# Performance work log

Measured on AMD Instinct MI355X. Metric: run time of the kernel, lower is better.

## Reference

```python
import jax, jax.numpy as jnp
import numpy as np

B, T, E, H = 256, 256, 64, 4  # batch, num_trees, embedding_size, hidden_size


def setup_inputs() -> dict:
    key = jax.random.key(0)
    k1, k2, k3 = jax.random.split(key, 3)
    x = jax.random.normal(k1, (B, 1, T, E), dtype=jnp.float32)
    W1 = jax.random.normal(k2, (T, T, E, H), dtype=jnp.float32) * 0.01  # linear1 (leading 1 dropped)
    b1 = jnp.zeros((T, T, H), dtype=jnp.float32)
    W2 = jax.random.normal(k3, (T, (T - 1) * H, E), dtype=jnp.float32) * 0.01  # linear2
    b2 = jnp.zeros((T, E), dtype=jnp.float32)
    return {"x": x, "W1": W1, "b1": b1, "W2": W2, "b2": b2}


def _offdiag_idx(num_trees):
    # For each output tree i, the column indices j != i (static, shape [T, T-1]).
    mask = ~np.eye(num_trees, dtype=bool)
    return jnp.asarray(np.nonzero(mask)[1].reshape(num_trees, num_trees - 1))


def reference(x, W1, b1, W2, b2):
    num_trees, hidden = W1.shape[0], W1.shape[-1]
    x0 = x[:, 0]  # (B, T, E): broadcast dim removed; x[b,0,j,e] pairs with W1[i,j,e,h]
    # Locally-connected layer 1: per-pair (i,j) contraction over embedding dim e.
    h = jax.nn.relu(jnp.einsum('bje,ijeh->bijh', x0, W1) + b1)  # (B, T, T, H)
    # Dropout(p=0.5) is identity in eval mode.
    # masked_select(~eye): drop the diagonal j == i via a static gather.
    idx = _offdiag_idx(num_trees)  # (T, T-1)
    h2 = jnp.take_along_axis(h, idx[None, :, :, None], axis=2)  # (B, T, T-1, H)
    h2 = h2.reshape(h.shape[0], num_trees, (num_trees - 1) * hidden)
    # Locally-connected layer 2: per-tree i contraction over the (T-1)*H dim.
    out = jnp.einsum('btk,tke->bte', h2, W2) + b2  # (B, T, E)
    return out
```

## Files before the change

kernel.cpp:

```cpp
#include <hip/hip_runtime.h>


namespace {

constexpr int T_ = 256;
constexpr int E_ = 64;
constexpr int K2_ = 1020;

typedef float  f32x4  __attribute__((ext_vector_type(4)));
typedef short  bf16x8 __attribute__((ext_vector_type(8)));
typedef unsigned short u16x4 __attribute__((ext_vector_type(4)));

__device__ inline unsigned short f2b(float f) {
    union { float f; unsigned u; } v; v.f = f;
    unsigned r = v.u + 0x7fffu + ((v.u >> 16) & 1u);
    return (unsigned short)(r >> 16);
}

__device__ inline bf16x8 pack8(f32x4 a, f32x4 b) {
    bf16x8 r;
    r[0] = (short)f2b(a[0]); r[1] = (short)f2b(a[1]);
    r[2] = (short)f2b(a[2]); r[3] = (short)f2b(a[3]);
    r[4] = (short)f2b(b[0]); r[5] = (short)f2b(b[1]);
    r[6] = (short)f2b(b[2]); r[7] = (short)f2b(b[3]);
    return r;
}

constexpr int JC = 4;
constexpr int CHUNKS = 16;
constexpr int W1_ROW   = 72;
constexpr int W1_PLANE = 32 * W1_ROW + 8;
constexpr int PB_ROW   = 24;
constexpr int PB_PLANE = 64 * PB_ROW + 8;
constexpr int W2_ROW   = 16;
constexpr int W2_PLANE = 64 * W2_ROW + 8;

}


__global__ __launch_bounds__(256) void xcast_kernel(
    const float* __restrict__ x, unsigned short* __restrict__ xT)
{
    const int g     = blockIdx.x * 256 + threadIdx.x;
    const int part  = g & 3;
    const int rowid = g >> 2;
    const int b = rowid >> 8, j = rowid & 255;
    const float* src = x + (size_t)rowid * E_ + part * 16;
    f32x4 v0 = *(const f32x4*)(src);
    f32x4 v1 = *(const f32x4*)(src + 4);
    f32x4 v2 = *(const f32x4*)(src + 8);
    f32x4 v3 = *(const f32x4*)(src + 12);
    unsigned short* dst = xT + ((size_t)j * 256 + b) * E_ + part * 16;
    *(bf16x8*)(dst)     = pack8(v0, v1);
    *(bf16x8*)(dst + 8) = pack8(v2, v3);
}

__global__ __launch_bounds__(256) void init_out_kernel(
    const float* __restrict__ b2, float* __restrict__ out)
{
    const int idx = blockIdx.x * 256 + threadIdx.x;
    ((f32x4*)out)[idx] = ((const f32x4*)b2)[idx & 4095];
}


__global__ __launch_bounds__(512, 2) void w2z_kernel(
    const float* __restrict__ W2, unsigned short* __restrict__ W2Z)
{
    __shared__ __align__(16) unsigned short sT[64][136];
    const int bid = blockIdx.x;
    const int t = bid >> 3, kb = bid & 7;
    const int tid = threadIdx.x;
    {
        const int kl = tid >> 2;
        const int e0 = (tid & 3) << 4;
        const int k  = kb * 128 + kl;
        const int j  = k >> 2, h = k & 3;
        f32x4 v0 = {0,0,0,0}, v1 = {0,0,0,0}, v2 = {0,0,0,0}, v3 = {0,0,0,0};
        if (j != t) {
            const int ksrc = ((j < t) ? j : j - 1) * 4 + h;
            const float* src = W2 + ((size_t)t * K2_ + ksrc) * E_ + e0;
            v0 = *(const f32x4*)(src);
            v1 = *(const f32x4*)(src + 4);
            v2 = *(const f32x4*)(src + 8);
            v3 = *(const f32x4*)(src + 12);
        }
        #pragma unroll
        for (int m = 0; m < 4; ++m) {
            sT[e0 + m     ][kl] = f2b(v0[m]);
            sT[e0 + 4 + m ][kl] = f2b(v1[m]);
            sT[e0 + 8 + m ][kl] = f2b(v2[m]);
            sT[e0 + 12 + m][kl] = f2b(v3[m]);
        }
    }
    __syncthreads();
    {
        const int e  = tid >> 3;
        const int ko = tid & 7;
        const unsigned short* srow = &sT[e][ko * 16];
        bf16x8 a = *(const bf16x8*)(srow);
        bf16x8 b = *(const bf16x8*)(srow + 8);
        unsigned short* dst = W2Z + ((size_t)t * 64 + e) * 1024 + kb * 128 + ko * 16;
        *(bf16x8*)(dst)     = a;
        *(bf16x8*)(dst + 8) = b;
    }
}

__global__ __launch_bounds__(256, 4) void phaseA4_kernel(
    const unsigned short* __restrict__ xT,
    const float* __restrict__ W1,
    const float* __restrict__ b1,
    unsigned short* __restrict__ H,
    int i_gbase)
{
    __shared__ __align__(16) unsigned short sA[4][2][16][68];
    __shared__ __align__(16) unsigned short sH[4][4][64][8];

    const int bx = blockIdx.x;
    const int jq = ((bx & 7) << 3) | (bx >> 3);
    const int it = blockIdx.y;
    const int bh = blockIdx.z;

    const int tid = threadIdx.x;
    const int w = tid >> 6, lane = tid & 63, r16 = lane & 15, kg = lane >> 4;
    const int jp = w & 1, bq = w >> 1;
    const int bG = bh * 128 + bq * 64;
    const int jbase = jq * 4 + jp * 2;

    bf16x8 xf[2][4][2];
    #pragma unroll
    for (int jl = 0; jl < 2; ++jl)
        #pragma unroll
        for (int nt = 0; nt < 4; ++nt) {
            const unsigned short* xr =
                xT + ((size_t)(jbase + jl) * 256 + bG + nt * 16 + r16) * 64 + kg * 8;
            xf[jl][nt][0] = *(const bf16x8*)(xr);
            xf[jl][nt][1] = *(const bf16x8*)(xr + 32);
        }

    const int s_jl = lane >> 5, s_il = (lane >> 3) & 3, s_seg = lane & 7;

    for (int iq = 0; iq < 4; ++iq) {
        {
            const int ig = i_gbase + it * 16 + iq * 4 + s_il;
            const float* src = W1 + (((size_t)ig * 256 + (jbase + s_jl)) << 8) + s_seg * 32;
            f32x4 v[8];
            #pragma unroll
            for (int s4 = 0; s4 < 8; ++s4) v[s4] = *(const f32x4*)(src + s4 * 4);
            #pragma unroll
            for (int h = 0; h < 4; ++h) {
                bf16x8 pk;
                #pragma unroll
                for (int s4 = 0; s4 < 8; ++s4) pk[s4] = (short)f2b(v[s4][h]);
                *(bf16x8*)&sA[w][s_jl][s_il * 4 + h][s_seg * 8] = pk;
            }
        }
        asm volatile("s_waitcnt lgkmcnt(0)" ::: "memory");
        __builtin_amdgcn_sched_barrier(0);

        {
            bf16x8 a[2][2];
            f32x4 bias[2];
            const int igk = i_gbase + it * 16 + iq * 4 + kg;
            #pragma unroll
            for (int jl = 0; jl < 2; ++jl) {
                const unsigned short* ar = &sA[w][jl][r16][0];
                a[jl][0] = *(const bf16x8*)(ar + kg * 8);
                a[jl][1] = *(const bf16x8*)(ar + 32 + kg * 8);
                bias[jl] = *(const f32x4*)(b1 + (((size_t)igk << 8) + (jbase + jl)) * 4);
            }
            #pragma unroll
            for (int nt = 0; nt < 4; ++nt) {
                unsigned pk[4];
                #pragma unroll
                for (int jl = 0; jl < 2; ++jl) {
                    f32x4 acc = (f32x4){0.f, 0.f, 0.f, 0.f};
                    acc = __builtin_amdgcn_mfma_f32_16x16x32_bf16(a[jl][0], xf[jl][nt][0], acc, 0, 0, 0);
                    acc = __builtin_amdgcn_mfma_f32_16x16x32_bf16(a[jl][1], xf[jl][nt][1], acc, 0, 0, 0);
                    float v0 = acc[0] + bias[jl][0]; v0 = v0 > 0.f ? v0 : 0.f;
                    float v1 = acc[1] + bias[jl][1]; v1 = v1 > 0.f ? v1 : 0.f;
                    float v2 = acc[2] + bias[jl][2]; v2 = v2 > 0.f ? v2 : 0.f;
                    float v3 = acc[3] + bias[jl][3]; v3 = v3 > 0.f ? v3 : 0.f;
                    pk[jl * 2]     = (unsigned)f2b(v0) | ((unsigned)f2b(v1) << 16);
                    pk[jl * 2 + 1] = (unsigned)f2b(v2) | ((unsigned)f2b(v3) << 16);
                }
                uint4 q4; q4.x = pk[0]; q4.y = pk[1]; q4.z = pk[2]; q4.w = pk[3];
                *(uint4*)&sH[w][kg][nt * 16 + r16][0] = q4;
            }
        }
        asm volatile("s_waitcnt lgkmcnt(0)" ::: "memory");
        __builtin_amdgcn_sched_barrier(0);

        {
            const int ib = it * 16 + iq * 4;
            #pragma unroll
            for (int il = 0; il < 4; ++il) {
                bf16x8 v = *(const bf16x8*)&sH[w][il][lane][0];
                *(bf16x8*)(H + (((((size_t)(ib + il)) * 64 + jq) * 2 + jp) * 256 + bG + lane) * 8) = v;
            }
        }
    }
}

__global__ __launch_bounds__(512, 4) void phaseB_kernel(
    const unsigned short* __restrict__ H,
    const unsigned short* __restrict__ W2Z,
    const float* __restrict__ b2,
    float* __restrict__ out,
    int i_base)
{
    __shared__ __align__(16) unsigned short sA[2][128][72];
    __shared__ __align__(16) unsigned short sB[2][64][72];

    const int bid = blockIdx.x;
    const int t_loc = bid >> 1;
    const int t  = i_base + t_loc;
    const int b0 = (bid & 1) << 7;
    const int tid = threadIdx.x;
    const int w = tid >> 6, lane = tid & 63, r16 = lane & 15, kg = lane >> 4;

    auto stageA = [&](int c, int pb) {
        #pragma unroll
        for (int half = 0; half < 2; ++half) {
            const int idx = half * 512 + tid;
            const int b   = idx & 127;
            const int jp  = (idx >> 7) & 1;
            const int jql = (idx >> 8) & 3;
            const unsigned short* src =
                H + ((size_t)t_loc << 18) +
                ((size_t)((((4 * c + jql) * 2 + jp) * 256) + b0 + b) << 3);
            bf16x8 v = *(const bf16x8*)src;
            *(bf16x8*)&sA[pb][b][jql * 16 + jp * 8] = v;
        }
    };
    auto stageB = [&](int c, int pb) {
        const int e = tid >> 3;
        const int q = tid & 7;
        bf16x8 v = *(const bf16x8*)(W2Z + ((size_t)t * 64 + e) * 1024 + c * 64 + q * 8);
        *(bf16x8*)&sB[pb][e][q * 8] = v;
    };

    stageA(0, 0); stageB(0, 0);
    __syncthreads();

    f32x4 acc[4];
    #pragma unroll
    for (int nt = 0; nt < 4; ++nt) acc[nt] = (f32x4){0.f, 0.f, 0.f, 0.f};

    for (int c = 0; c < 16; ++c) {
        const int pb = c & 1;
        if (c + 1 < 16) { stageA(c + 1, pb ^ 1); stageB(c + 1, pb ^ 1); }

        const unsigned short* ar = &sA[pb][w * 16 + r16][0];
        bf16x8 a0 = *(const bf16x8*)(ar + kg * 8);
        bf16x8 a1 = *(const bf16x8*)(ar + 32 + kg * 8);
        #pragma unroll
        for (int nt = 0; nt < 4; ++nt) {
            const unsigned short* br = &sB[pb][nt * 16 + r16][0];
            bf16x8 bb0 = *(const bf16x8*)(br + kg * 8);
            bf16x8 bb1 = *(const bf16x8*)(br + 32 + kg * 8);
            acc[nt] = __builtin_amdgcn_mfma_f32_16x16x32_bf16(a0, bb0, acc[nt], 0, 0, 0);
            acc[nt] = __builtin_amdgcn_mfma_f32_16x16x32_bf16(a1, bb1, acc[nt], 0, 0, 0);
        }
        __syncthreads();
    }

    #pragma unroll
    for (int nt = 0; nt < 4; ++nt) {
        const int e = nt * 16 + r16;
        const float bias = b2[(t << 6) + e];
        #pragma unroll
        for (int r = 0; r < 4; ++r) {
            const int b = b0 + w * 16 + kg * 4 + r;
            out[((size_t)b << 14) + (t << 6) + e] = acc[nt][r] + bias;
        }
    }
}


template <bool XBF>
__global__ __launch_bounds__(512, 4) void fused_forest_kernel(
    const void*  __restrict__ xv,
    const float* __restrict__ W1,
    const float* __restrict__ b1,
    const float* __restrict__ W2,
    float* __restrict__ out)
{
    __shared__ __align__(16) unsigned short sW1[4 * W1_PLANE];
    __shared__ __align__(16) unsigned short sPB[8 * PB_PLANE];
    __shared__ __align__(16) unsigned short sW2[2][8 * W2_PLANE];
    __shared__ __align__(16) float sB1[4][32];

    const int bid = blockIdx.x;
    const int xcd = bid & 7;
    const int rr  = bid >> 3;
    const int tgl = rr >> 4;
    const int bg  = (rr >> 2) & 3;
    const int jg  = rr & 3;
    const int tg  = tgl * 8 + xcd;
    const int i0  = tg << 3;
    const int b0  = bg << 6;
    const int j0g = jg << 6;

    const int tid  = threadIdx.x;
    const int w    = tid >> 6;
    const int lane = tid & 63;
    const int r16  = lane & 15;
    const int kg   = lane >> 4;
    const int bt   = w & 3;
    const int mh   = w >> 2;

    f32x4 acc[4][4];
    #pragma unroll
    for (int mt = 0; mt < 4; ++mt)
        #pragma unroll
        for (int nt = 0; nt < 4; ++nt)
            acc[mt][nt] = (f32x4){0.f, 0.f, 0.f, 0.f};

    auto stage = [&](int c, int pb) {
        const int j0 = j0g + c * JC;
        if (tid < 128) {
            const int jj = tid >> 5, ih = tid & 31;
            sB1[jj][ih] = b1[((i0 + (ih >> 2)) * T_ + (j0 + jj)) * 4 + (ih & 3)];
        }
        {
            const float* src = W1 + (((size_t)(i0 + w) * T_ + (j0 + kg)) * E_) * 4 + r16 * 16;
            f32x4 v0 = *(const f32x4*)(src);
            f32x4 v1 = *(const f32x4*)(src + 4);
            f32x4 v2 = *(const f32x4*)(src + 8);
            f32x4 v3 = *(const f32x4*)(src + 12);
            #pragma unroll
            for (int h = 0; h < 4; ++h) {
                u16x4 pk = (u16x4){f2b(v0[h]), f2b(v1[h]), f2b(v2[h]), f2b(v3[h])};
                *(u16x4*)&sW1[kg * W1_PLANE + (w * 4 + h) * W1_ROW + r16 * 4] = pk;
            }
        }
        {
            const int kk   = lane >> 2;
            const int e0   = (lane & 3) * 16;
            const int tabs = i0 + w;
            const int j    = j0 + (kk >> 2);
            unsigned short* dst = &sW2[pb][w * W2_PLANE + kk];
            if (j == tabs) {
                #pragma unroll
                for (int q = 0; q < 16; ++q) dst[(e0 + q) * W2_ROW] = 0;
            } else {
                const int ksrc = ((j < tabs) ? j : j - 1) * 4 + (kk & 3);
                const float* src = W2 + ((size_t)tabs * K2_ + ksrc) * E_ + e0;
                f32x4 v0 = *(const f32x4*)(src);
                f32x4 v1 = *(const f32x4*)(src + 4);
                f32x4 v2 = *(const f32x4*)(src + 8);
                f32x4 v3 = *(const f32x4*)(src + 12);
                #pragma unroll
                for (int q = 0; q < 4; ++q) {
                    dst[(e0 + q)      * W2_ROW] = f2b(v0[q]);
                    dst[(e0 + 4 + q)  * W2_ROW] = f2b(v1[q]);
                    dst[(e0 + 8 + q)  * W2_ROW] = f2b(v2[q]);
                    dst[(e0 + 12 + q) * W2_ROW] = f2b(v3[q]);
                }
            }
        }
    };

    stage(0, 0);
    __syncthreads();

    const int brow = b0 + bt * 16 + r16;

    for (int c = 0; c < CHUNKS; ++c) {
        const int j0 = j0g + c * JC;
        #pragma unroll
        for (int jj = 0; jj < JC; ++jj) {
            bf16x8 xa, xc;
            if (XBF) {
                const unsigned short* xr =
                    (const unsigned short*)xv + ((size_t)(j0 + jj) * 256 + brow) * E_;
                xa = *(const bf16x8*)(xr + kg * 8);
                xc = *(const bf16x8*)(xr + 32 + kg * 8);
            } else {
                const float* xr = (const float*)xv + ((size_t)brow * T_ + (j0 + jj)) * E_ + kg * 8;
                xa = pack8(*(const f32x4*)xr, *(const f32x4*)(xr + 4));
                xc = pack8(*(const f32x4*)(xr + 32), *(const f32x4*)(xr + 36));
            }
            const unsigned short* wr = &sW1[jj * W1_PLANE + (mh * 16 + r16) * W1_ROW];
            bf16x8 wa = *(const bf16x8*)(wr + kg * 8);
            bf16x8 wc = *(const bf16x8*)(wr + 32 + kg * 8);
            f32x4 cf = (f32x4){0.f, 0.f, 0.f, 0.f};
            cf = __builtin_amdgcn_mfma_f32_16x16x32_bf16(wa, xa, cf, 0, 0, 0);
            cf = __builtin_amdgcn_mfma_f32_16x16x32_bf16(wc, xc, cf, 0, 0, 0);
            const int i = mh * 4 + kg;
            f32x4 bias = *(const f32x4*)&sB1[jj][i * 4];
            #pragma unroll
            for (int r = 0; r < 4; ++r) {
                float vv = cf[r] + bias[r];
                cf[r] = vv > 0.f ? vv : 0.f;
            }
            unsigned p0 = (unsigned)f2b(cf[0]) | ((unsigned)f2b(cf[1]) << 16);
            unsigned p1 = (unsigned)f2b(cf[2]) | ((unsigned)f2b(cf[3]) << 16);
            uint2 pk; pk.x = p0; pk.y = p1;
            *(uint2*)&sPB[i * PB_PLANE + (bt * 16 + r16) * PB_ROW + jj * 4] = pk;
        }
        __syncthreads();

        {
            const bf16x8 z = (bf16x8){0,0,0,0,0,0,0,0};
            const bool lo = (kg < 2);
            bf16x8 a2[4], bb[4];
            #pragma unroll
            for (int mt = 0; mt < 4; ++mt)
                a2[mt] = lo ? *(const bf16x8*)&sPB[w * PB_PLANE + (mt * 16 + r16) * PB_ROW + kg * 8] : z;
            #pragma unroll
            for (int nt = 0; nt < 4; ++nt)
                bb[nt] = lo ? *(const bf16x8*)&sW2[c & 1][w * W2_PLANE + (nt * 16 + r16) * W2_ROW + kg * 8] : z;
            #pragma unroll
            for (int mt = 0; mt < 4; ++mt)
                #pragma unroll
                for (int nt = 0; nt < 4; ++nt)
                    acc[mt][nt] = __builtin_amdgcn_mfma_f32_16x16x32_bf16(
                        a2[mt], bb[nt], acc[mt][nt], 0, 0, 0);
        }

        if (c + 1 < CHUNKS) stage(c + 1, (c + 1) & 1);
        __syncthreads();
    }

    const int tabs = i0 + w;
    #pragma unroll
    for (int mt = 0; mt < 4; ++mt) {
        const int b = b0 + mt * 16 + kg * 4;
        #pragma unroll
        for (int nt = 0; nt < 4; ++nt) {
            const int e = nt * 16 + r16;
            #pragma unroll
            for (int r = 0; r < 4; ++r)
                unsafeAtomicAdd(&out[((size_t)(b + r) * T_ + tabs) * E_ + e],
                                acc[mt][nt][r]);
        }
    }
}


extern "C" void kernel_launch(void* const* d_in, const int* in_sizes, int n_in,
                              void* d_out, int out_size, void* d_ws, size_t ws_size,
                              hipStream_t stream) {
    const float* x  = (const float*)d_in[0];
    const float* W1 = (const float*)d_in[1];
    const float* b1 = (const float*)d_in[2];
    const float* W2 = (const float*)d_in[3];
    const float* b2 = (const float*)d_in[4];
    float* out = (float*)d_out;
    (void)in_sizes; (void)n_in; (void)out_size;

    const size_t xT_b   = 8388608ull;
    const size_t w2z_b  = 33554432ull;
    const size_t H_full = 134217728ull;

    int NS = 0;
    if (d_ws) {
        const int cands[4] = {1, 2, 4, 8};
        for (int ci = 0; ci < 4; ++ci) {
            if (ws_size >= xT_b + w2z_b + H_full / cands[ci]) { NS = cands[ci]; break; }
        }
    }

    if (NS) {
        unsigned short* xT  = (unsigned short*)d_ws;
        unsigned short* W2Z = (unsigned short*)((char*)d_ws + xT_b);
        unsigned short* H   = (unsigned short*)((char*)d_ws + xT_b + w2z_b);

        hipLaunchKernelGGL(xcast_kernel, dim3(1024), dim3(256), 0, stream, x, xT);
        hipLaunchKernelGGL(w2z_kernel, dim3(2048), dim3(512), 0, stream, W2, W2Z);

        const int TS = 256 / NS;
        const int n_it = TS / 16;
        for (int s = 0; s < NS; ++s) {
            hipLaunchKernelGGL(phaseA4_kernel, dim3(64, n_it, 2), dim3(256), 0, stream,
                               xT, W1, b1, H, s * TS);
            hipLaunchKernelGGL(phaseB_kernel, dim3(TS * 2), dim3(512), 0, stream,
                               H, W2Z, b2, out, s * TS);
        }
    } else {
        const bool xbf = d_ws && ws_size >= xT_b;
        hipLaunchKernelGGL(init_out_kernel, dim3(4096), dim3(256), 0, stream, b2, out);
        if (xbf) {
            hipLaunchKernelGGL(xcast_kernel, dim3(1024), dim3(256), 0, stream,
                               x, (unsigned short*)d_ws);
            hipLaunchKernelGGL(fused_forest_kernel<true>, dim3(512), dim3(512), 0, stream,
                               (const void*)d_ws, W1, b1, W2, out);
        } else {
            hipLaunchKernelGGL(fused_forest_kernel<false>, dim3(512), dim3(512), 0, stream,
                               (const void*)x, W1, b1, W2, out);
        }
    }
}
```

Measured before the change: 128.8 us.

## Share W1 tile across waves with double-buffered LDS and prefetch in phase A

Phase A now loads each W1 block into a shared LDS buffer used by all four waves, instead of each wave loading its own copy. It double-buffers that buffer and issues the next iq's global loads before the MFMA work, so load latency overlaps compute. Bias is staged once in LDS, and H is written straight from registers, dropping the sH staging round-trip. In exchange it adds block-wide barriers each iteration and writes H with a less coalesced pattern.

```diff
diff --git a/kernel.cpp b/kernel.cpp
--- a/kernel.cpp
+++ b/kernel.cpp
@@ -105,26 +105,32 @@
     }
 }
 
-__global__ __launch_bounds__(256, 4) void phaseA4_kernel(
+__global__ __launch_bounds__(256, 4) void phaseA6_kernel(
     const unsigned short* __restrict__ xT,
     const float* __restrict__ W1,
     const float* __restrict__ b1,
     unsigned short* __restrict__ H,
     int i_gbase)
 {
-    __shared__ __align__(16) unsigned short sA[4][2][16][68];
-    __shared__ __align__(16) unsigned short sH[4][4][64][8];
+    __shared__ __align__(16) unsigned short sA[2][4][16][72];
+    __shared__ __align__(16) float sB1[16][16];
 
     const int bx = blockIdx.x;
     const int jq = ((bx & 7) << 3) | (bx >> 3);
     const int it = blockIdx.y;
     const int bh = blockIdx.z;
+    const int j0 = jq * 4;
 
     const int tid = threadIdx.x;
     const int w = tid >> 6, lane = tid & 63, r16 = lane & 15, kg = lane >> 4;
     const int jp = w & 1, bq = w >> 1;
     const int bG = bh * 128 + bq * 64;
-    const int jbase = jq * 4 + jp * 2;
+    const int jbase = j0 + jp * 2;
+
+    {
+        const int i = tid >> 4, f = tid & 15;
+        sB1[i][f] = b1[(((size_t)(i_gbase + it * 16 + i)) * 256 + j0) * 4 + f];
+    }
 
     bf16x8 xf[2][4][2];
     #pragma unroll
@@ -137,37 +143,47 @@
             xf[jl][nt][1] = *(const bf16x8*)(xr + 32);
         }
 
-    const int s_jl = lane >> 5, s_il = (lane >> 3) & 3, s_seg = lane & 7;
-
+    const int p_s = tid >> 4, seg = tid & 15;
+    const int il_s = p_s >> 2, jW = p_s & 3;
+
+    f32x4 r[4];
+    auto issue = [&](int iq) {
+        const float* src = W1 +
+            ((((size_t)(i_gbase + it * 16 + iq * 4 + il_s)) * 256 + (j0 + jW)) << 8) + seg * 16;
+        #pragma unroll
+        for (int s = 0; s < 4; ++s) r[s] = *(const f32x4*)(src + s * 4);
+    };
+    auto packwrite = [&](int buf) {
+        #pragma unroll
+        for (int h = 0; h < 4; ++h) {
+            u16x4 pk = (u16x4){f2b(r[0][h]), f2b(r[1][h]), f2b(r[2][h]), f2b(r[3][h])};
+            *(u16x4*)&sA[buf][jW][il_s * 4 + h][seg * 4] = pk;
+        }
+    };
+
+    issue(0);
+    packwrite(0);
+    issue(1);
+    asm volatile("s_waitcnt lgkmcnt(0)" ::: "memory");
+    __builtin_amdgcn_sched_barrier(0);
+    __builtin_amdgcn_s_barrier();
+    __builtin_amdgcn_sched_barrier(0);
+
+    #pragma unroll
     for (int iq = 0; iq < 4; ++iq) {
-        {
-            const int ig = i_gbase + it * 16 + iq * 4 + s_il;
-            const float* src = W1 + (((size_t)ig * 256 + (jbase + s_jl)) << 8) + s_seg * 32;
-            f32x4 v[8];
-            #pragma unroll
-            for (int s4 = 0; s4 < 8; ++s4) v[s4] = *(const f32x4*)(src + s4 * 4);
-            #pragma unroll
-            for (int h = 0; h < 4; ++h) {
-                bf16x8 pk;
-                #pragma unroll
-                for (int s4 = 0; s4 < 8; ++s4) pk[s4] = (short)f2b(v[s4][h]);
-                *(bf16x8*)&sA[w][s_jl][s_il * 4 + h][s_seg * 8] = pk;
-            }
-        }
-        asm volatile("s_waitcnt lgkmcnt(0)" ::: "memory");
-        __builtin_amdgcn_sched_barrier(0);
+        const int buf = iq & 1;
 
         {
             bf16x8 a[2][2];
             f32x4 bias[2];
-            const int igk = i_gbase + it * 16 + iq * 4 + kg;
             #pragma unroll
             for (int jl = 0; jl < 2; ++jl) {
-                const unsigned short* ar = &sA[w][jl][r16][0];
+                const unsigned short* ar = &sA[buf][jp * 2 + jl][r16][0];
                 a[jl][0] = *(const bf16x8*)(ar + kg * 8);
                 a[jl][1] = *(const bf16x8*)(ar + 32 + kg * 8);
-                bias[jl] = *(const f32x4*)(b1 + (((size_t)igk << 8) + (jbase + jl)) * 4);
+                bias[jl] = *(const f32x4*)&sB1[iq * 4 + kg][(jp * 2 + jl) * 4];
             }
+            const size_t iR = it * 16 + iq * 4 + kg;
             #pragma unroll
             for (int nt = 0; nt < 4; ++nt) {
                 unsigned pk[4];
@@ -184,19 +200,17 @@
                     pk[jl * 2 + 1] = (unsigned)f2b(v2) | ((unsigned)f2b(v3) << 16);
                 }
                 uint4 q4; q4.x = pk[0]; q4.y = pk[1]; q4.z = pk[2]; q4.w = pk[3];
-                *(uint4*)&sH[w][kg][nt * 16 + r16][0] = q4;
+                *(uint4*)(H + (((((size_t)iR) * 64 + jq) * 2 + jp) * 256 + bG + nt * 16 + r16) * 8) = q4;
             }
         }
-        asm volatile("s_waitcnt lgkmcnt(0)" ::: "memory");
-        __builtin_amdgcn_sched_barrier(0);
-
-        {
-            const int ib = it * 16 + iq * 4;
-            #pragma unroll
-            for (int il = 0; il < 4; ++il) {
-                bf16x8 v = *(const bf16x8*)&sH[w][il][lane][0];
-                *(bf16x8*)(H + (((((size_t)(ib + il)) * 64 + jq) * 2 + jp) * 256 + bG + lane) * 8) = v;
-            }
+
+        if (iq < 3) {
+            packwrite(buf ^ 1);
+            if (iq < 2) issue(iq + 2);
+            asm volatile("s_waitcnt lgkmcnt(0)" ::: "memory");
+            __builtin_amdgcn_sched_barrier(0);
+            __builtin_amdgcn_s_barrier();
+            __builtin_amdgcn_sched_barrier(0);
         }
     }
 }
@@ -473,7 +487,7 @@
         const int TS = 256 / NS;
         const int n_it = TS / 16;
         for (int s = 0; s < NS; ++s) {
-            hipLaunchKernelGGL(phaseA4_kernel, dim3(64, n_it, 2), dim3(256), 0, stream,
+            hipLaunchKernelGGL(phaseA6_kernel, dim3(64, n_it, 2), dim3(256), 0, stream,
                                xT, W1, b1, H, s * TS);
             hipLaunchKernelGGL(phaseB_kernel, dim3(TS * 2), dim3(512), 0, stream,
                                H, W2Z, b2, out, s * TS);
```

Measured after the change: 154.8 us. 1.2x slower.
